# Optimization experiments

Measured on AMD Instinct MI355X. Metric: run time of the kernel, lower is better.

The kernel has to match this reference:

```python
import jax, jax.numpy as jnp
import numpy as np

N_NODES = 5000
N_EDGES = 80000
IN_DIM = 128
HID_DIM = 128
OUT_DIM = 64
NUM_HEADS = 1
BATCH = 8
NEG_SLOPE = 0.2  # DGL GATConv default leaky_relu negative_slope


def setup_inputs() -> dict:
    key = jax.random.key(0)
    ks = jax.random.split(key, 12)
    x = jax.random.normal(ks[0], (BATCH, N_NODES, IN_DIM), dtype=jnp.float32)
    src = jax.random.randint(ks[1], (N_EDGES,), 0, N_NODES)
    dst = jax.random.randint(ks[2], (N_EDGES,), 0, N_NODES)
    # layer1 params (fc has no bias in DGL GATConv; output bias present by default)
    s1 = 1.0 / np.sqrt(IN_DIM)
    W1 = jax.random.normal(ks[3], (IN_DIM, NUM_HEADS * HID_DIM), dtype=jnp.float32) * s1
    al1 = jax.random.normal(ks[4], (NUM_HEADS, HID_DIM), dtype=jnp.float32) * 0.1
    ar1 = jax.random.normal(ks[5], (NUM_HEADS, HID_DIM), dtype=jnp.float32) * 0.1
    b1 = jnp.zeros((NUM_HEADS * HID_DIM,), dtype=jnp.float32)
    # layer2 params
    s2 = 1.0 / np.sqrt(NUM_HEADS * HID_DIM)
    W2 = jax.random.normal(ks[6], (NUM_HEADS * HID_DIM, NUM_HEADS * OUT_DIM), dtype=jnp.float32) * s2
    al2 = jax.random.normal(ks[7], (NUM_HEADS, OUT_DIM), dtype=jnp.float32) * 0.1
    ar2 = jax.random.normal(ks[8], (NUM_HEADS, OUT_DIM), dtype=jnp.float32) * 0.1
    b2 = jnp.zeros((NUM_HEADS * OUT_DIM,), dtype=jnp.float32)
    return {"x": x, "W1": W1, "al1": al1, "ar1": ar1, "b1": b1,
            "W2": W2, "al2": al2, "ar2": ar2, "b2": b2,
            "src": src, "dst": dst}


def gat_layer(x, W, al, ar, b, src, dst, n_nodes):
    """DGL GATConv. x:[B,N,Din] W:[Din,H*F] al/ar:[H,F] b:[H*F] -> [B,N,H,F]."""
    B = x.shape[0]
    H, F = al.shape
    z = (x @ W).reshape(B, n_nodes, H, F)                 # [B,N,H,F]
    el = jnp.einsum('bnhf,hf->bnh', z, al)                # src-side attn term
    er = jnp.einsum('bnhf,hf->bnh', z, ar)                # dst-side attn term
    e = jax.nn.leaky_relu(el[:, src] + er[:, dst], NEG_SLOPE)  # [B,E,H]
    e = jnp.moveaxis(e, 1, 0)                             # [E,B,H]  edge-major for segment ops
    emax = jax.ops.segment_max(e, dst, num_segments=n_nodes)   # [N,B,H]
    ex = jnp.exp(e - emax[dst])
    denom = jax.ops.segment_sum(ex, dst, num_segments=n_nodes)  # [N,B,H]
    alpha = ex / denom[dst]                               # edge softmax over incoming edges
    zs = jnp.moveaxis(z[:, src], 1, 0)                    # [E,B,H,F] gathered source feats
    out = jax.ops.segment_sum(alpha[..., None] * zs, dst, num_segments=n_nodes)  # [N,B,H,F]
    return jnp.moveaxis(out, 0, 1) + b.reshape(1, 1, H, F)


def reference(x, W1, al1, ar1, b1, W2, al2, ar2, b2, src, dst):
    n_nodes = x.shape[1]
    h = gat_layer(x, W1, al1, ar1, b1, src, dst, n_nodes)  # [B,N,H,hid]
    B, N, H, Fh = h.shape
    h = h.reshape(B, N, H * Fh)                            # concat heads (H=1)
    o = gat_layer(h, W2, al2, ar2, b2, src, dst, n_nodes)  # [B,N,H,out]
    o = o.reshape(B * N, -1)                               # squeeze: [B*N, out]
    return jax.nn.softmax(o, axis=-1)
```

## Files before the change

kernel.cpp:

```cpp
#include <hip/hip_runtime.h>
#include <hip/hip_bf16.h>

#define N_NODES 5000
#define N_EDGES 80000
#define HID_DIM 128
#define OUT_DIM 64
#define BATCH 8
#define M_ROWS 40000
#define NEG_SLOPE 0.2f
#define BUCKET 96


typedef unsigned short ushort_t;
typedef unsigned int uint_t;
typedef __attribute__((ext_vector_type(8))) short short8;
typedef __attribute__((ext_vector_type(4))) float f32x4;

__device__ __forceinline__ float bf16_to_f32(ushort_t u) {
  return __uint_as_float(((uint_t)u) << 16);
}
__device__ __forceinline__ ushort_t f32_to_bf16(float f) {
  uint_t u = __float_as_uint(f);
  return (ushort_t)((u + 0x7FFF + ((u >> 16) & 1)) >> 16);
}

#define OFF_CMETA 49152u
#define OFF_CB    49184u
#define OFF_Y     65536u
#define OFF_EY    5185536u
#define OFF_W     5505536u
#define OFF_EL1   10625536u
#define OFF_ER1   10785536u
#define OFF_EL2   10945536u
#define OFF_ER2   11105536u
#define OFF_CNT   11265536u
#define OFF_SRCS  11285536u

__global__ __launch_bounds__(256) void gemm_fused(const float* __restrict__ A,
                                                  const float* __restrict__ W1,
                                                  const float* __restrict__ W2,
                                                  const float* __restrict__ b1,
                                                  const float* __restrict__ b2,
                                                  const float* __restrict__ al1,
                                                  const float* __restrict__ ar1,
                                                  const float* __restrict__ al2,
                                                  const float* __restrict__ ar2,
                                                  float* __restrict__ el1,
                                                  float* __restrict__ er1,
                                                  ushort_t* __restrict__ y,
                                                  float2* __restrict__ ey,
                                                  const int* __restrict__ e_src,
                                                  const int* __restrict__ e_dst,
                                                  int* __restrict__ cnt,
                                                  int* __restrict__ srcs,
                                                  float* __restrict__ cmeta,
                                                  float* __restrict__ cb) {
  __shared__ ushort_t ldsB1[2048 * 8];
  __shared__ ushort_t ldsB2[1024 * 8];
  __shared__ ushort_t lds[64 * 128];
  int wave = threadIdx.x >> 6, lane = threadIdx.x & 63;
  int q = lane >> 4, m = lane & 15;
  int r0 = blockIdx.x * 64 + wave * 16;

  if (threadIdx.x < 128) {
    int i = blockIdx.x * 128 + threadIdx.x;
    int d = e_dst[i];
    int pos = atomicAdd(&cnt[d], 1);
    if (pos < BUCKET) srcs[d * BUCKET + pos] = e_src[i];
  }

  for (int it = 0; it < 12; it++) {
    int gid = it * 256 + threadIdx.x;
    const float* W; ushort_t* Bp; int NC, idx;
    if (gid < 2048) { W = W1; Bp = ldsB1; NC = 128; idx = gid; }
    else            { W = W2; Bp = ldsB2; NC = 64;  idx = gid - 2048; }
    int l = idx & 63, tt = idx >> 6;
    int T = NC / 16;
    int kc = tt / T, t = tt % T;
    int col = t * 16 + (l & 15);
    int krow = kc * 32 + (l >> 4) * 8;
    short8 vv;
#pragma unroll
    for (int j = 0; j < 8; j++) vv[j] = (short)f32_to_bf16(W[(size_t)(krow + j) * NC + col]);
    *(short8*)(Bp + (size_t)idx * 8) = vv;
  }

  if (blockIdx.x == 0 && threadIdx.x < 64) {
    int f = threadIdx.x;
    float c = 0.f;
#pragma unroll 8
    for (int k = 0; k < 128; k++) c += b1[k] * W2[(size_t)k * 64 + f];
    cb[f] = c + b2[f];
    float cl = c * al2[f], cr = c * ar2[f];
#pragma unroll
    for (int o = 32; o; o >>= 1) {
      cl += __shfl_xor(cl, o, 64);
      cr += __shfl_xor(cr, o, 64);
    }
    if (f == 0) { cmeta[0] = cl; cmeta[1] = cr; }
  }
  __syncthreads();

  f32x4 acc[8];
#pragma unroll
  for (int t = 0; t < 8; t++)
#pragma unroll
    for (int i = 0; i < 4; i++) acc[t][i] = 0.f;
  const short8* B1 = (const short8*)ldsB1;
  size_t arow = (size_t)(r0 + m) * 128;
#pragma unroll
  for (int kc = 0; kc < 4; kc++) {
    const float* Ap = A + arow + kc * 32 + q * 8;
    float4 v0 = *(const float4*)Ap;
    float4 v1 = *(const float4*)(Ap + 4);
    short8 af;
    af[0] = (short)f32_to_bf16(v0.x); af[1] = (short)f32_to_bf16(v0.y);
    af[2] = (short)f32_to_bf16(v0.z); af[3] = (short)f32_to_bf16(v0.w);
    af[4] = (short)f32_to_bf16(v1.x); af[5] = (short)f32_to_bf16(v1.y);
    af[6] = (short)f32_to_bf16(v1.z); af[7] = (short)f32_to_bf16(v1.w);
#pragma unroll
    for (int t = 0; t < 8; t++)
      acc[t] = __builtin_amdgcn_mfma_f32_16x16x32_bf16(af, B1[(kc * 8 + t) * 64 + lane], acc[t], 0, 0, 0);
  }
  {
    float sl[4] = {0.f, 0.f, 0.f, 0.f}, sr[4] = {0.f, 0.f, 0.f, 0.f};
#pragma unroll
    for (int t = 0; t < 8; t++) {
      float alv = al1[t * 16 + m], arv = ar1[t * 16 + m];
#pragma unroll
      for (int i = 0; i < 4; i++) { sl[i] += acc[t][i] * alv; sr[i] += acc[t][i] * arv; }
    }
#pragma unroll
    for (int o = 1; o < 16; o <<= 1)
#pragma unroll
      for (int i = 0; i < 4; i++) {
        sl[i] += __shfl_xor(sl[i], o, 64);
        sr[i] += __shfl_xor(sr[i], o, 64);
      }
    if (m == 0)
#pragma unroll
      for (int i = 0; i < 4; i++) {
        el1[r0 + q * 4 + i] = sl[i];
        er1[r0 + q * 4 + i] = sr[i];
      }
  }
#pragma unroll
  for (int t = 0; t < 8; t++)
#pragma unroll
    for (int i = 0; i < 4; i++) {
      int row = q * 4 + i + wave * 16;
      int byte = row * 256 + (t * 16 + m) * 2;
      lds[(byte ^ ((row & 7) << 4)) >> 1] = f32_to_bf16(acc[t][i]);
    }
  __syncthreads();

  f32x4 acc2[4];
#pragma unroll
  for (int t = 0; t < 4; t++)
#pragma unroll
    for (int i = 0; i < 4; i++) acc2[t][i] = 0.f;
  const short8* B2 = (const short8*)ldsB2;
  int row2 = wave * 16 + m;
#pragma unroll
  for (int kc = 0; kc < 4; kc++) {
    int byte = row2 * 256 + kc * 64 + q * 16;
    short8 af2 = *(const short8*)((const char*)lds + (byte ^ ((row2 & 7) << 4)));
#pragma unroll
    for (int t = 0; t < 4; t++)
      acc2[t] = __builtin_amdgcn_mfma_f32_16x16x32_bf16(af2, B2[(kc * 4 + t) * 64 + lane], acc2[t], 0, 0, 0);
  }
  {
    float sl[4] = {0.f, 0.f, 0.f, 0.f}, sr[4] = {0.f, 0.f, 0.f, 0.f};
#pragma unroll
    for (int t = 0; t < 4; t++) {
      float alv = al2[t * 16 + m], arv = ar2[t * 16 + m];
#pragma unroll
      for (int i = 0; i < 4; i++) { sl[i] += acc2[t][i] * alv; sr[i] += acc2[t][i] * arv; }
    }
#pragma unroll
    for (int o = 1; o < 16; o <<= 1)
#pragma unroll
      for (int i = 0; i < 4; i++) {
        sl[i] += __shfl_xor(sl[i], o, 64);
        sr[i] += __shfl_xor(sr[i], o, 64);
      }
    if (m == 0)
#pragma unroll
      for (int i = 0; i < 4; i++) ey[r0 + q * 4 + i] = make_float2(sl[i], sr[i]);
  }
#pragma unroll
  for (int t = 0; t < 4; t++)
#pragma unroll
    for (int i = 0; i < 4; i++)
      y[(size_t)(r0 + q * 4 + i) * 64 + t * 16 + m] = f32_to_bf16(acc2[t][i]);
}

__global__ __launch_bounds__(256) void agg_mid(const ushort_t* __restrict__ y,
                                               const float2* __restrict__ ey,
                                               const float* __restrict__ el,
                                               const float* __restrict__ er,
                                               const int* __restrict__ cnt,
                                               const int* __restrict__ srcs,
                                               const float* __restrict__ cmeta,
                                               ushort_t* __restrict__ w,
                                               float* __restrict__ el2,
                                               float* __restrict__ er2) {
  int id = (threadIdx.x >> 6) * gridDim.x + blockIdx.x;
  int lane = threadIdx.x & 63;
  int g = lane >> 4, l16 = lane & 15;
  int b = id & 7, n = id >> 3;
  int deg = cnt[n]; if (deg > BUCKET) deg = BUCKET;
  int off0 = n * BUCKET;
  int rbase = b * N_NODES;
  float er_n = er[rbase + n];

  float acc[4] = {0.f, 0.f, 0.f, 0.f};
  float lsum = 0.f, sl2 = 0.f, sr2 = 0.f;

  for (int c = 0; c < deg; c += 64) {
    int j = c + lane;
    int s_my = 0;
    float w_my = 0.f;
    if (j < deg) {
      s_my = srcs[off0 + j];
      float e = el[rbase + s_my] + er_n;
      e = e > 0.f ? e : NEG_SLOPE * e;
      w_my = __expf(e);
      lsum += w_my;
      float2 ev = ey[rbase + s_my];
      sl2 += w_my * ev.x;
      sr2 += w_my * ev.y;
    }
    int cl = deg - c; if (cl > 64) cl = 64;
    for (int k0 = 0; k0 < cl; k0 += 16) {
      float wk[4]; int sk[4];
#pragma unroll
      for (int u = 0; u < 4; u++) {
        int e_idx = k0 + u * 4 + g;
        wk[u] = __shfl(w_my, e_idx, 64);
        sk[u] = __shfl(s_my, e_idx, 64);
      }
      uint2 zw[4];
#pragma unroll
      for (int u = 0; u < 4; u++)
        zw[u] = *(const uint2*)(y + (size_t)(rbase + sk[u]) * 64 + l16 * 4);
#pragma unroll
      for (int u = 0; u < 4; u++) {
        acc[0] += wk[u] * bf16_to_f32((ushort_t)(zw[u].x & 0xFFFF));
        acc[1] += wk[u] * bf16_to_f32((ushort_t)(zw[u].x >> 16));
        acc[2] += wk[u] * bf16_to_f32((ushort_t)(zw[u].y & 0xFFFF));
        acc[3] += wk[u] * bf16_to_f32((ushort_t)(zw[u].y >> 16));
      }
    }
  }
#pragma unroll
  for (int j = 0; j < 4; j++) {
    acc[j] += __shfl_xor(acc[j], 16, 64);
    acc[j] += __shfl_xor(acc[j], 32, 64);
  }
  float sum = lsum;
#pragma unroll
  for (int o = 32; o; o >>= 1) {
    sum += __shfl_xor(sum, o, 64);
    sl2 += __shfl_xor(sl2, o, 64);
    sr2 += __shfl_xor(sr2, o, 64);
  }
  float inv = (deg > 0) ? 1.f / sum : 0.f;

  if (g == 0) {
    uint_t pk0 = (uint_t)f32_to_bf16(acc[0] * inv) | ((uint_t)f32_to_bf16(acc[1] * inv) << 16);
    uint_t pk1 = (uint_t)f32_to_bf16(acc[2] * inv) | ((uint_t)f32_to_bf16(acc[3] * inv) << 16);
    *(uint2*)(w + (size_t)(rbase + n) * 64 + l16 * 4) = make_uint2(pk0, pk1);
  }
  if (lane == 0) {
    el2[rbase + n] = sl2 * inv + cmeta[0];
    er2[rbase + n] = sr2 * inv + cmeta[1];
  }
}

__global__ __launch_bounds__(256) void agg_fin(const ushort_t* __restrict__ w,
                                               const float* __restrict__ el,
                                               const float* __restrict__ er,
                                               const float* __restrict__ cb,
                                               const int* __restrict__ cnt,
                                               const int* __restrict__ srcs,
                                               float* __restrict__ outp) {
  int id = (threadIdx.x >> 6) * gridDim.x + blockIdx.x;
  int lane = threadIdx.x & 63;
  int g = lane >> 4, l16 = lane & 15;
  int b = id & 7, n = id >> 3;
  int deg = cnt[n]; if (deg > BUCKET) deg = BUCKET;
  int off0 = n * BUCKET;
  int rbase = b * N_NODES;
  float er_n = er[rbase + n];

  float acc[4] = {0.f, 0.f, 0.f, 0.f};
  float lsum = 0.f;

  for (int c = 0; c < deg; c += 64) {
    int j = c + lane;
    int s_my = 0;
    float w_my = 0.f;
    if (j < deg) {
      s_my = srcs[off0 + j];
      float e = el[rbase + s_my] + er_n;
      e = e > 0.f ? e : NEG_SLOPE * e;
      w_my = __expf(e);
      lsum += w_my;
    }
    int cl = deg - c; if (cl > 64) cl = 64;
    for (int k0 = 0; k0 < cl; k0 += 16) {
      float wk[4]; int sk[4];
#pragma unroll
      for (int u = 0; u < 4; u++) {
        int e_idx = k0 + u * 4 + g;
        wk[u] = __shfl(w_my, e_idx, 64);
        sk[u] = __shfl(s_my, e_idx, 64);
      }
      uint2 zw[4];
#pragma unroll
      for (int u = 0; u < 4; u++)
        zw[u] = *(const uint2*)(w + (size_t)(rbase + sk[u]) * 64 + l16 * 4);
#pragma unroll
      for (int u = 0; u < 4; u++) {
        acc[0] += wk[u] * bf16_to_f32((ushort_t)(zw[u].x & 0xFFFF));
        acc[1] += wk[u] * bf16_to_f32((ushort_t)(zw[u].x >> 16));
        acc[2] += wk[u] * bf16_to_f32((ushort_t)(zw[u].y & 0xFFFF));
        acc[3] += wk[u] * bf16_to_f32((ushort_t)(zw[u].y >> 16));
      }
    }
  }
#pragma unroll
  for (int j = 0; j < 4; j++) {
    acc[j] += __shfl_xor(acc[j], 16, 64);
    acc[j] += __shfl_xor(acc[j], 32, 64);
  }
  float sum = lsum;
#pragma unroll
  for (int o = 32; o; o >>= 1) sum += __shfl_xor(sum, o, 64);
  float inv = (deg > 0) ? 1.f / sum : 0.f;

  float o[4];
#pragma unroll
  for (int j = 0; j < 4; j++) o[j] = acc[j] * inv + cb[l16 * 4 + j];
  float mm = fmaxf(fmaxf(o[0], o[1]), fmaxf(o[2], o[3]));
#pragma unroll
  for (int d = 1; d < 16; d <<= 1) mm = fmaxf(mm, __shfl_xor(mm, d, 64));
  float p0 = __expf(o[0] - mm), p1 = __expf(o[1] - mm);
  float p2 = __expf(o[2] - mm), p3 = __expf(o[3] - mm);
  float ss = p0 + p1 + p2 + p3;
#pragma unroll
  for (int d = 1; d < 16; d <<= 1) ss += __shfl_xor(ss, d, 64);
  if (g == 0) {
    float issv = 1.f / ss;
    *(float4*)(outp + (size_t)(rbase + n) * 64 + l16 * 4) =
        make_float4(p0 * issv, p1 * issv, p2 * issv, p3 * issv);
  }
}

extern "C" void kernel_launch(void* const* d_in, const int* in_sizes, int n_in,
                              void* d_out, int out_size, void* d_ws, size_t ws_size,
                              hipStream_t stream) {
  const float* x   = (const float*)d_in[0];
  const float* W1  = (const float*)d_in[1];
  const float* al1 = (const float*)d_in[2];
  const float* ar1 = (const float*)d_in[3];
  const float* b1  = (const float*)d_in[4];
  const float* W2  = (const float*)d_in[5];
  const float* al2 = (const float*)d_in[6];
  const float* ar2 = (const float*)d_in[7];
  const float* b2  = (const float*)d_in[8];
  const int* src = (const int*)d_in[9];
  const int* dst = (const int*)d_in[10];

  char* base = (char*)d_ws;
  float*    cmeta= (float*)(base + OFF_CMETA);
  float*    cb   = (float*)(base + OFF_CB);
  ushort_t* y    = (ushort_t*)(base + OFF_Y);
  float2*   ey   = (float2*)(base + OFF_EY);
  ushort_t* w    = (ushort_t*)(base + OFF_W);
  float* el1 = (float*)(base + OFF_EL1);
  float* er1 = (float*)(base + OFF_ER1);
  float* el2 = (float*)(base + OFF_EL2);
  float* er2 = (float*)(base + OFF_ER2);
  int* cnt  = (int*)(base + OFF_CNT);
  int* srcs = (int*)(base + OFF_SRCS);

  hipMemsetAsync(cnt, 0, N_NODES * sizeof(int), stream);

  gemm_fused<<<M_ROWS / 64, 256, 0, stream>>>(x, W1, W2, b1, b2, al1, ar1, al2, ar2,
                                              el1, er1, y, ey, src, dst, cnt, srcs,
                                              cmeta, cb);

  agg_mid<<<M_ROWS / 4, 256, 0, stream>>>(y, ey, el1, er1, cnt, srcs, cmeta, w, el2, er2);

  agg_fin<<<M_ROWS / 4, 256, 0, stream>>>(w, el2, er2, cb, cnt, srcs, (float*)d_out);
}
```

Measured before the change: 146.8 us.

## Build CSR buckets in LDS-owned node ranges and drop memset

Replaces the per-block global atomic bucketing of edges with 20 owner blocks, each scanning all edges and counting its own 250-node range with LDS atomics, then writing counts to global memory. This removes the separate hipMemsetAsync launch and the contended global atomics. In exchange, each of the 20 owner blocks reads all 80k edges serially before starting its GEMM tile, which can make those blocks stragglers. The cmeta/cb computation moves to block 20.

```diff
diff --git a/kernel.cpp b/kernel.cpp
--- a/kernel.cpp
+++ b/kernel.cpp
@@ -35,6 +35,8 @@
 #define OFF_ER2   11105536u
 #define OFF_CNT   11265536u
 #define OFF_SRCS  11285536u
+
+#define NODES_PER_OWNER 250
 
 __global__ __launch_bounds__(256) void gemm_fused(const float* __restrict__ A,
                                                   const float* __restrict__ W1,
@@ -58,19 +60,14 @@
   __shared__ ushort_t ldsB1[2048 * 8];
   __shared__ ushort_t ldsB2[1024 * 8];
   __shared__ ushort_t lds[64 * 128];
-  int wave = threadIdx.x >> 6, lane = threadIdx.x & 63;
+  int* cnt_lds = (int*)lds;
+  int tid = threadIdx.x, bid = blockIdx.x;
+  int wave = tid >> 6, lane = tid & 63;
   int q = lane >> 4, m = lane & 15;
-  int r0 = blockIdx.x * 64 + wave * 16;
-
-  if (threadIdx.x < 128) {
-    int i = blockIdx.x * 128 + threadIdx.x;
-    int d = e_dst[i];
-    int pos = atomicAdd(&cnt[d], 1);
-    if (pos < BUCKET) srcs[d * BUCKET + pos] = e_src[i];
-  }
+  int r0 = bid * 64 + wave * 16;
 
   for (int it = 0; it < 12; it++) {
-    int gid = it * 256 + threadIdx.x;
+    int gid = it * 256 + tid;
     const float* W; ushort_t* Bp; int NC, idx;
     if (gid < 2048) { W = W1; Bp = ldsB1; NC = 128; idx = gid; }
     else            { W = W2; Bp = ldsB2; NC = 64;  idx = gid - 2048; }
@@ -85,8 +82,25 @@
     *(short8*)(Bp + (size_t)idx * 8) = vv;
   }
 
-  if (blockIdx.x == 0 && threadIdx.x < 64) {
-    int f = threadIdx.x;
+  if (bid < 20) {
+    int base = bid * NODES_PER_OWNER;
+    if (tid < NODES_PER_OWNER) cnt_lds[tid] = 0;
+    __syncthreads();
+    for (int j = tid; j < N_EDGES; j += 256) {
+      int d = e_dst[j];
+      int s = e_src[j];
+      int rel = d - base;
+      if ((unsigned)rel < (unsigned)NODES_PER_OWNER) {
+        int pos = atomicAdd(&cnt_lds[rel], 1);
+        if (pos < BUCKET) srcs[d * BUCKET + pos] = s;
+      }
+    }
+    __syncthreads();
+    if (tid < NODES_PER_OWNER) cnt[base + tid] = cnt_lds[tid];
+  }
+
+  if (bid == 20 && tid < 64) {
+    int f = tid;
     float c = 0.f;
 #pragma unroll 8
     for (int k = 0; k < 128; k++) c += b1[k] * W2[(size_t)k * 64 + f];
@@ -386,8 +400,6 @@
   int* cnt  = (int*)(base + OFF_CNT);
   int* srcs = (int*)(base + OFF_SRCS);
 
-  hipMemsetAsync(cnt, 0, N_NODES * sizeof(int), stream);
-
   gemm_fused<<<M_ROWS / 64, 256, 0, stream>>>(x, W1, W2, b1, b2, al1, ar1, al2, ar2,
                                               el1, er1, y, ey, src, dst, cnt, srcs,
                                               cmeta, cb);
```

Result: slower. 300.5 us (+104.8%).
